# Kernel optimization log

Hardware: AMD Instinct MI355X
Metric: run time of the kernel (lower is better)

Reference implementation:

```python
import jax, jax.numpy as jnp
import numpy as np

N_ACC = 100000   # accounts
N_TX = 300000    # transactions
E = 600000       # edges per edge type
H = 256          # hidden_dim
TX_IN = 32
ACC_IN = 16
L = 2            # conv_layers
M = 300000       # edges to classify
BN_EPS = 1e-5


def setup_inputs() -> dict:
    key = jax.random.key(0)
    ks = jax.random.split(key, 24)
    def nrm(k, shape, scale=1.0):
        return jax.random.normal(k, shape, jnp.float32) * scale
    inp = {}
    inp["x_acc"] = nrm(ks[0], (N_ACC, ACC_IN))
    inp["x_tx"] = nrm(ks[1], (N_TX, TX_IN))
    inp["tx_raw"] = nrm(ks[2], (M, TX_IN))
    # edge type account -> transaction (row0: src account, row1: dst transaction)
    inp["ei_sends"] = jnp.stack([jax.random.randint(ks[3], (E,), 0, N_ACC),
                                 jax.random.randint(ks[4], (E,), 0, N_TX)])
    # edge type transaction -> account
    inp["ei_recv"] = jnp.stack([jax.random.randint(ks[5], (E,), 0, N_TX),
                                jax.random.randint(ks[6], (E,), 0, N_ACC)])
    inp["sender_idx"] = jax.random.randint(ks[7], (M,), 0, N_ACC)
    inp["receiver_idx"] = jax.random.randint(ks[8], (M,), 0, N_ACC)
    # input projections (torch Linear: y = x @ W.T + b)
    inp["W_acc"] = nrm(ks[9], (H, ACC_IN), ACC_IN ** -0.5)
    inp["b_acc"] = jnp.zeros((H,), jnp.float32)
    inp["W_tx"] = nrm(ks[10], (H, TX_IN), TX_IN ** -0.5)
    inp["b_tx"] = jnp.zeros((H,), jnp.float32)
    s = H ** -0.5
    # SAGEConv params per layer: _at = acc->tx edge type, _ta = tx->acc edge type
    # Wl: applied to mean-aggregated neighbor messages (has bias), Wr: root/self weight (no bias)
    inp["Wl_at"] = nrm(ks[11], (L, H, H), s); inp["bl_at"] = jnp.zeros((L, H), jnp.float32)
    inp["Wr_at"] = nrm(ks[12], (L, H, H), s)
    inp["Wl_ta"] = nrm(ks[13], (L, H, H), s); inp["bl_ta"] = jnp.zeros((L, H), jnp.float32)
    inp["Wr_ta"] = nrm(ks[14], (L, H, H), s)
    # shared BatchNorm1d per layer (inference mode: running stats)
    inp["bn_gamma"] = jnp.ones((L, H), jnp.float32)
    inp["bn_beta"] = jnp.zeros((L, H), jnp.float32)
    inp["bn_mean"] = nrm(ks[15], (L, H), 0.1)
    inp["bn_var"] = jax.random.uniform(ks[16], (L, H), jnp.float32, 0.5, 1.5)
    # edge MLP: Linear(2H+TX_IN -> H), ReLU, Linear(H -> 1)
    inp["W1"] = nrm(ks[17], (H, 2 * H + TX_IN), (2 * H + TX_IN) ** -0.5)
    inp["b1"] = jnp.zeros((H,), jnp.float32)
    inp["W2"] = nrm(ks[18], (1, H), s)
    inp["b2"] = jnp.zeros((1,), jnp.float32)
    return inp


def _sage(x_src, x_dst, ei, Wl, bl, Wr):
    # PyG SAGEConv: lin_l(mean_{j in N(i)} x_src[j]) + lin_r(x_dst[i])
    src, dst = ei[0], ei[1]
    n_dst = x_dst.shape[0]
    msg = x_src[src]                                                   # [E, H] gather
    agg = jax.ops.segment_sum(msg, dst, num_segments=n_dst)           # [N_dst, H] scatter-add
    cnt = jax.ops.segment_sum(jnp.ones((ei.shape[1],), x_src.dtype), dst, num_segments=n_dst)
    mean = agg / jnp.maximum(cnt, 1.0)[:, None]
    return mean @ Wl.T + bl + x_dst @ Wr.T


def _bn(v, g, b, m, var):
    return (v - m) * (g * jax.lax.rsqrt(var + BN_EPS)) + b


def reference(x_acc, x_tx, tx_raw, ei_sends, ei_recv, sender_idx, receiver_idx,
              W_acc, b_acc, W_tx, b_tx,
              Wl_at, bl_at, Wr_at, Wl_ta, bl_ta, Wr_ta,
              bn_gamma, bn_beta, bn_mean, bn_var,
              W1, b1, W2, b2):
    acc = jax.nn.relu(x_acc @ W_acc.T + b_acc)
    tx = jax.nn.relu(x_tx @ W_tx.T + b_tx)
    for l in range(L):
        # HeteroConv(aggr='sum'): each node type receives from exactly one edge type here
        tx_new = _sage(acc, tx, ei_sends, Wl_at[l], bl_at[l], Wr_at[l])
        acc_new = _sage(tx, acc, ei_recv, Wl_ta[l], bl_ta[l], Wr_ta[l])
        acc = jax.nn.relu(_bn(acc_new, bn_gamma[l], bn_beta[l], bn_mean[l], bn_var[l]))
        tx = jax.nn.relu(_bn(tx_new, bn_gamma[l], bn_beta[l], bn_mean[l], bn_var[l]))
    h_sender = acc[sender_idx]      # [M, H]
    h_receiver = acc[receiver_idx]  # [M, H]
    edge_repr = jnp.concatenate([h_sender, h_receiver, tx_raw], axis=1)  # [M, 2H+TX_IN]
    h = jax.nn.relu(edge_repr @ W1.T + b1)
    return (h @ W2.T + b2)[:, 0]    # [M]
```

## Files before the change

### kernel.cpp

```cpp
#include <hip/hip_runtime.h>
#include <hip/hip_bf16.h>

#define H 256
#define NACC 100000
#define NTX  300000
#define NE   600000
#define NM   300000

typedef unsigned short u16;
typedef unsigned int u32;
typedef __bf16 bf16x8 __attribute__((ext_vector_type(8)));
typedef float f32x4 __attribute__((ext_vector_type(4)));

__device__ __forceinline__ float bf2f(u32 u) {
    union { u32 i; float f; } v; v.i = u << 16; return v.f;
}
__device__ __forceinline__ u16 f2bf(float f) {
    union { float f; u32 i; } v; v.f = f;
    u32 r = v.i + 0x7FFFu + ((v.i >> 16) & 1u);
    return (u16)(r >> 16);
}
__device__ __forceinline__ u32 pk2(float a, float b) {
    return (u32)f2bf(a) | ((u32)f2bf(b) << 16);
}

__global__ void fillz_kernel(u32* __restrict__ p, long long n) {
    long long i = (long long)blockIdx.x * blockDim.x + threadIdx.x;
    long long st = (long long)gridDim.x * blockDim.x;
    for (; i < n; i += st) p[i] = 0u;
}

__global__ void wcat_kernel(const float* __restrict__ Wl, const float* __restrict__ Wr,
                            u16* __restrict__ dst) {
    int c = blockIdx.x, t = threadIdx.x;
    dst[(size_t)c * 512 + t]       = f2bf(Wl[(size_t)c * 256 + t]);
    dst[(size_t)c * 512 + 256 + t] = f2bf(Wr[(size_t)c * 256 + t]);
}
__global__ void wcat_frag_kernel(const float* __restrict__ Wl, const float* __restrict__ Wr,
                                 u16* __restrict__ dst) {
    int c = blockIdx.x, k = threadIdx.x;
    float v = (k < 256) ? Wl[(size_t)c * 256 + k] : Wr[(size_t)c * 256 + (k - 256)];
    int kstep = k >> 5, kg = (k & 31) >> 3, j = k & 7;
    dst[(size_t)((kstep * 16 + (c >> 4)) * 64 + kg * 16 + (c & 15)) * 8 + j] = f2bf(v);
}
__global__ void w1frag_kernel(const float* __restrict__ W1, u16* __restrict__ dst) {
    int c = blockIdx.x;
    for (int k = threadIdx.x; k < 544; k += 256) {
        float v = W1[(size_t)c * 544 + k];
        int kstep = k >> 5, kg = (k & 31) >> 3, j = k & 7;
        dst[(size_t)((kstep * 16 + (c >> 4)) * 64 + kg * 16 + (c & 15)) * 8 + j] = f2bf(v);
    }
}
__global__ void wproj_kernel(const float* __restrict__ W, u16* __restrict__ dst, int K) {
    int c = blockIdx.x, t = threadIdx.x;
    dst[(size_t)c * 32 + t] = (t < K) ? f2bf(W[(size_t)c * K + t]) : (u16)0;
}
__global__ void bnprep_kernel(const float* __restrict__ bl, const float* __restrict__ g,
                              const float* __restrict__ be, const float* __restrict__ m,
                              const float* __restrict__ v,
                              float* __restrict__ S, float* __restrict__ B) {
    int c = threadIdx.x;
    float s = g[c] * rsqrtf(v[c] + 1e-5f);
    S[c] = s;
    B[c] = (bl[c] - m[c]) * s + be[c];
}

template <int KK>
__launch_bounds__(256)
__global__ void proj_mfma(const float* __restrict__ x, const u16* __restrict__ Wb,
                          const float* __restrict__ b, u16* __restrict__ out, int N) {
    __shared__ __align__(16) u16 Af[8][64][8];
    __shared__ __align__(16) u16 Bf[16][64][8];
    int tid = threadIdx.x;
    int w = tid >> 6, lane = tid & 63;
    int row0 = blockIdx.x * 128;
    {
        int r = tid >> 1, h = tid & 1;
        int gr = row0 + r;
        int rt = r >> 4, rr = r & 15;
        uint4 p0 = make_uint4(0, 0, 0, 0), p1 = p0;
        if (gr < N && (KK == 32 || h == 0)) {
            const float* xp = x + (size_t)gr * KK + h * 16;
            float4 f0 = *(const float4*)(xp);
            float4 f1 = *(const float4*)(xp + 4);
            float4 f2 = *(const float4*)(xp + 8);
            float4 f3 = *(const float4*)(xp + 12);
            p0 = make_uint4(pk2(f0.x, f0.y), pk2(f0.z, f0.w), pk2(f1.x, f1.y), pk2(f1.z, f1.w));
            p1 = make_uint4(pk2(f2.x, f2.y), pk2(f2.z, f2.w), pk2(f3.x, f3.y), pk2(f3.z, f3.w));
        }
        int kg0 = 2 * h;
        *(uint4*)(&Af[rt][(kg0 * 16 + rr) ^ (kg0 << 2)][0]) = p0;
        *(uint4*)(&Af[rt][((kg0 + 1) * 16 + rr) ^ ((kg0 + 1) << 2)][0]) = p1;
    }
    {
        const u16* wp = Wb + (size_t)tid * 32;
#pragma unroll
        for (int q = 0; q < 4; ++q) {
            uint4 wv = *(const uint4*)(wp + q * 8);
            *(uint4*)(&Bf[tid >> 4][q * 16 + (tid & 15)][0]) = wv;
        }
    }
    __syncthreads();
    int arslot = lane ^ ((lane >> 4) << 2);
    f32x4 acc[8][4];
#pragma unroll
    for (int rt = 0; rt < 8; ++rt) {
        bf16x8 afr = *(const bf16x8*)(&Af[rt][arslot][0]);
#pragma unroll
        for (int ct = 0; ct < 4; ++ct) {
            bf16x8 bfr = *(const bf16x8*)(&Bf[w * 4 + ct][lane][0]);
            acc[rt][ct] = __builtin_amdgcn_mfma_f32_16x16x32_bf16(
                afr, bfr, (f32x4){0.f, 0.f, 0.f, 0.f}, 0, 0, 0);
        }
    }
    int rb = (lane >> 4) * 4, cc = lane & 15;
#pragma unroll
    for (int ct = 0; ct < 4; ++ct) {
        int cg = (w * 4 + ct) * 16 + cc;
        float bv = b[cg];
#pragma unroll
        for (int rt = 0; rt < 8; ++rt)
#pragma unroll
            for (int q = 0; q < 4; ++q) {
                int r = row0 + rt * 16 + rb + q;
                if (r < N)
                    out[(size_t)r * H + cg] = f2bf(fmaxf(acc[rt][ct][q] + bv, 0.0f));
            }
    }
}

__global__ void count_kernel(const int* __restrict__ dst, int E, int* __restrict__ cnt) {
    int e = blockIdx.x * blockDim.x + threadIdx.x;
    if (e < E) atomicAdd(&cnt[dst[e]], 1);
}
__global__ void scan1_kernel(const int* __restrict__ cnt, int N,
                             int* __restrict__ loc, int* __restrict__ bsum) {
    __shared__ int sh[256];
    int b = blockIdx.x, t = threadIdx.x;
    int base = b * 1024 + t * 4;
    int v0 = (base + 0 < N) ? cnt[base + 0] : 0;
    int v1 = (base + 1 < N) ? cnt[base + 1] : 0;
    int v2 = (base + 2 < N) ? cnt[base + 2] : 0;
    int v3 = (base + 3 < N) ? cnt[base + 3] : 0;
    int s = v0 + v1 + v2 + v3;
    sh[t] = s;
    __syncthreads();
    for (int o = 1; o < 256; o <<= 1) {
        int y = (t >= o) ? sh[t - o] : 0;
        __syncthreads();
        sh[t] += y;
        __syncthreads();
    }
    int run = sh[t] - s;
    if (base + 0 < N) loc[base + 0] = run; run += v0;
    if (base + 1 < N) loc[base + 1] = run; run += v1;
    if (base + 2 < N) loc[base + 2] = run; run += v2;
    if (base + 3 < N) loc[base + 3] = run;
    if (t == 0) bsum[b] = sh[255];
}
__global__ void scan2_kernel(int* __restrict__ bsum, int nb) {
    __shared__ int sh[1024];
    int t = threadIdx.x;
    int v = (t < nb) ? bsum[t] : 0;
    sh[t] = v;
    __syncthreads();
    for (int o = 1; o < 1024; o <<= 1) {
        int y = (t >= o) ? sh[t - o] : 0;
        __syncthreads();
        sh[t] += y;
        __syncthreads();
    }
    if (t < nb) bsum[t] = sh[t] - v;
}
__global__ void scan3_kernel(int* __restrict__ ptr, const int* __restrict__ bsum,
                             int N, int total) {
    int i = blockIdx.x * blockDim.x + threadIdx.x;
    if (i < N) ptr[i] += bsum[i >> 10];
    else if (i == N) ptr[N] = total;
}
__global__ void fillcsr_kernel(const int* __restrict__ src, const int* __restrict__ dst, int E,
                               const int* __restrict__ ptr, int* __restrict__ cur,
                               int* __restrict__ perm) {
    int e = blockIdx.x * blockDim.x + threadIdx.x;
    if (e < E) {
        int d = dst[e];
        int pos = ptr[d] + atomicAdd(&cur[d], 1);
        perm[pos] = src[e];
    }
}

template <int WS>
__launch_bounds__(256)
__global__ void gmean_kernel(const u16* __restrict__ feat, int fstride,
                             const int* __restrict__ ptr, const int* __restrict__ perm,
                             u16* __restrict__ out, int ostride, int c0,
                             int rows, int lo) {
    constexpr int LPD = WS / 4;
    constexpr int DPB = 256 / LPD;
    int g = threadIdx.x / LPD;
    int ln = threadIdx.x % LPD;
    int w = blockIdx.x * DPB + g;
    if (w >= rows) return;
    int d = lo + w;
    int e0 = ptr[d], e1 = ptr[d + 1];
    float a0 = 0.f, a1 = 0.f, a2 = 0.f, a3 = 0.f;
    for (int e = e0; e < e1; ++e) {
        int s = perm[e];
        uint2 v = *(const uint2*)(feat + (size_t)s * fstride + (ln << 2));
        a0 += bf2f(v.x & 0xffff); a1 += bf2f(v.x >> 16);
        a2 += bf2f(v.y & 0xffff); a3 += bf2f(v.y >> 16);
    }
    int deg = e1 - e0;
    float sc = (deg > 0) ? (1.0f / (float)deg) : 0.0f;
    uint2 pk;
    pk.x = pk2(a0 * sc, a1 * sc);
    pk.y = pk2(a2 * sc, a3 * sc);
    *(uint2*)(out + (size_t)w * ostride + c0 + (ln << 2)) = pk;
}

template <int K, int NC>
__launch_bounds__(256)
__global__ void proj2_kernel(const float* __restrict__ x, const float* __restrict__ W,
                             const float* __restrict__ b, u16* __restrict__ out,
                             int N, int c0, int ost) {
    __shared__ float xs[128][K + 4];
    constexpr int NG = 512 / NC;
    constexpr int RPT = 128 / NG;
    int tid = threadIdx.x;
    int row0 = blockIdx.x * 128;
    constexpr int NF4 = 128 * K / 4;
    for (int f = tid; f < NF4; f += 256) {
        int r = f / (K / 4), kq = (f % (K / 4)) * 4;
        int gr = row0 + r;
        float4 v = (gr < N) ? *(const float4*)(x + (size_t)gr * K + kq)
                            : make_float4(0.f, 0.f, 0.f, 0.f);
        *(float4*)&xs[r][kq] = v;
    }
    int lt2 = (tid % (NC / 2)) * 2;
    int g = tid / (NC / 2);
    float wa[K], wb[K];
    const float* wpa = W + (size_t)(c0 + lt2) * K;
#pragma unroll
    for (int k = 0; k < K; k += 4) {
        float4 va = *(const float4*)(wpa + k);
        float4 vb = *(const float4*)(wpa + K + k);
        wa[k] = va.x; wa[k + 1] = va.y; wa[k + 2] = va.z; wa[k + 3] = va.w;
        wb[k] = vb.x; wb[k + 1] = vb.y; wb[k + 2] = vb.z; wb[k + 3] = vb.w;
    }
    float b0 = b[c0 + lt2], b1 = b[c0 + lt2 + 1];
    __syncthreads();
#pragma unroll
    for (int rr = 0; rr < RPT; ++rr) {
        int r = g * RPT + rr;
        int gr = row0 + r;
        float a0 = b0, a1 = b1;
#pragma unroll
        for (int k = 0; k < K; k += 4) {
            float4 xv = *(const float4*)&xs[r][k];
            a0 += xv.x * wa[k] + xv.y * wa[k + 1] + xv.z * wa[k + 2] + xv.w * wa[k + 3];
            a1 += xv.x * wb[k] + xv.y * wb[k + 1] + xv.z * wb[k + 2] + xv.w * wb[k + 3];
        }
        if (gr < N) {
            u32 pk = (u32)f2bf(fmaxf(a0, 0.f)) | ((u32)f2bf(fmaxf(a1, 0.f)) << 16);
            *(u32*)(out + (size_t)gr * ost + lt2) = pk;
        }
    }
}

__launch_bounds__(256)
__global__ void combine_gather(const u16* __restrict__ featG, const int* __restrict__ ptr,
                               const int* __restrict__ perm, const u16* __restrict__ xd,
                               const u16* __restrict__ WcF,
                               const float* __restrict__ bnS, const float* __restrict__ bnB,
                               u16* __restrict__ outF, int rows) {
    __shared__ __align__(16) u16 Am[8][4][64][8];
    int tid = threadIdx.x;
    int w = tid >> 6, lane = tid & 63;
    int row0 = blockIdx.x * 64;

    {
        int r = tid >> 2, g = tid & 3;
        int grow = row0 + r;
        float s[64];
#pragma unroll
        for (int i = 0; i < 64; ++i) s[i] = 0.0f;
        float inv = 0.0f;
        if (grow < rows) {
            int e0 = ptr[grow], e1 = ptr[grow + 1];
            int dg = e1 - e0;
            inv = (dg > 0) ? 1.0f / (float)dg : 0.0f;
            int e = e0;
            for (; e + 1 < e1; e += 2) {
                int n0 = perm[e], n1 = perm[e + 1];
                const u16* p0 = featG + (size_t)n0 * H + g * 64;
                const u16* p1 = featG + (size_t)n1 * H + g * 64;
#pragma unroll
                for (int q = 0; q < 8; ++q) {
                    uint4 v0 = *(const uint4*)(p0 + q * 8);
                    uint4 v1 = *(const uint4*)(p1 + q * 8);
                    s[q * 8 + 0] += bf2f(v0.x & 0xffff) + bf2f(v1.x & 0xffff);
                    s[q * 8 + 1] += bf2f(v0.x >> 16)    + bf2f(v1.x >> 16);
                    s[q * 8 + 2] += bf2f(v0.y & 0xffff) + bf2f(v1.y & 0xffff);
                    s[q * 8 + 3] += bf2f(v0.y >> 16)    + bf2f(v1.y >> 16);
                    s[q * 8 + 4] += bf2f(v0.z & 0xffff) + bf2f(v1.z & 0xffff);
                    s[q * 8 + 5] += bf2f(v0.z >> 16)    + bf2f(v1.z >> 16);
                    s[q * 8 + 6] += bf2f(v0.w & 0xffff) + bf2f(v1.w & 0xffff);
                    s[q * 8 + 7] += bf2f(v0.w >> 16)    + bf2f(v1.w >> 16);
                }
            }
            if (e < e1) {
                int n0 = perm[e];
                const u16* p0 = featG + (size_t)n0 * H + g * 64;
#pragma unroll
                for (int q = 0; q < 8; ++q) {
                    uint4 v0 = *(const uint4*)(p0 + q * 8);
                    s[q * 8 + 0] += bf2f(v0.x & 0xffff);
                    s[q * 8 + 1] += bf2f(v0.x >> 16);
                    s[q * 8 + 2] += bf2f(v0.y & 0xffff);
                    s[q * 8 + 3] += bf2f(v0.y >> 16);
                    s[q * 8 + 4] += bf2f(v0.z & 0xffff);
                    s[q * 8 + 5] += bf2f(v0.z >> 16);
                    s[q * 8 + 6] += bf2f(v0.w & 0xffff);
                    s[q * 8 + 7] += bf2f(v0.w >> 16);
                }
            }
        }
        int rt = r >> 4, rr = r & 15;
#pragma unroll
        for (int q = 0; q < 8; ++q) {
            int kgg = g * 8 + q;
            int kbs = kgg >> 2, akg = kgg & 3;
            uint4 pv;
            pv.x = pk2(s[q * 8 + 0] * inv, s[q * 8 + 1] * inv);
            pv.y = pk2(s[q * 8 + 2] * inv, s[q * 8 + 3] * inv);
            pv.z = pk2(s[q * 8 + 4] * inv, s[q * 8 + 5] * inv);
            pv.w = pk2(s[q * 8 + 6] * inv, s[q * 8 + 7] * inv);
            *(uint4*)(&Am[kbs][rt][(akg * 16 + rr) ^ (akg << 2)][0]) = pv;
        }
    }
    __syncthreads();

    int arslot = lane ^ ((lane >> 4) << 2);
    const u16* xrow[4];
#pragma unroll
    for (int rt = 0; rt < 4; ++rt) {
        int r = row0 + rt * 16 + (lane & 15);
        if (r > rows - 1) r = rows - 1;
        xrow[rt] = xd + (size_t)r * H + (lane >> 4) * 8;
    }
    const u16* wbase = WcF + (size_t)(w * 4) * 512 + (size_t)lane * 8;

    f32x4 acc[4][4];
#pragma unroll
    for (int i = 0; i < 4; ++i)
#pragma unroll
        for (int j = 0; j < 4; ++j) acc[i][j] = (f32x4){0.f, 0.f, 0.f, 0.f};

#pragma unroll 4
    for (int kb = 0; kb < 512; kb += 32) {
        int kstep = kb >> 5;
        bf16x8 afr[4];
        if (kb < 256) {
#pragma unroll
            for (int rt = 0; rt < 4; ++rt)
                afr[rt] = *(const bf16x8*)(&Am[kstep][rt][arslot][0]);
        } else {
#pragma unroll
            for (int rt = 0; rt < 4; ++rt)
                afr[rt] = *(const bf16x8*)(xrow[rt] + (kb - 256));
        }
#pragma unroll
        for (int ct = 0; ct < 4; ++ct) {
            bf16x8 bfr = *(const bf16x8*)(wbase + (size_t)(kstep * 16 + ct) * 512);
#pragma unroll
            for (int rt = 0; rt < 4; ++rt)
                acc[rt][ct] = __builtin_amdgcn_mfma_f32_16x16x32_bf16(afr[rt], bfr, acc[rt][ct], 0, 0, 0);
        }
    }
    __syncthreads();
    int rb = (lane >> 4) * 4, cc = lane & 15;
#pragma unroll
    for (int ct = 0; ct < 4; ++ct) {
        int cg = (w * 4 + ct) * 16 + cc;
        float s = bnS[cg], sh = bnB[cg];
#pragma unroll
        for (int rt = 0; rt < 4; ++rt)
#pragma unroll
            for (int q = 0; q < 4; ++q) {
                int r = row0 + rt * 16 + rb + q;
                if (r < rows)
                    outF[(size_t)r * H + cg] = f2bf(fmaxf(acc[rt][ct][q] * s + sh, 0.0f));
            }
    }
}

template <int COLS>
__launch_bounds__(256)
__global__ void combine_mfma(const u16* __restrict__ mean_, const u16* __restrict__ xd,
                             const u16* __restrict__ Wcat,
                             const float* __restrict__ bnS, const float* __restrict__ bnB,
                             u16* __restrict__ outF, int ostride, int out_c0,
                             int rows, int c0) {
    constexpr int NCT = COLS / 16;
    constexpr int CTW = NCT / 4;
    constexpr int PPT = (COLS * 4) / 256;
    __shared__ __align__(16) u16 Af[4][64][8];
    __shared__ __align__(16) u16 Bf[NCT][64][8];
    int tid = threadIdx.x;
    int w = tid >> 6, lane = tid & 63;
    int row0 = blockIdx.x * 64;
    int arow = tid >> 2, akg = tid & 3;
    bool arok = (row0 + arow) < rows;
    const u16* am = mean_ + (size_t)(row0 + arow) * H;
    const u16* ax = xd + (size_t)(row0 + arow) * H;
    int awslot = (akg * 16 + (arow & 15)) ^ (akg << 2);
    int arslot = lane ^ ((lane >> 4) << 2);
    int bc = tid % COLS;
    int bkg0 = (tid / COLS) * PPT;
    const u16* wp0 = Wcat + (size_t)(c0 + bc) * 512 + bkg0 * 8;

    f32x4 acc[4][CTW];
#pragma unroll
    for (int i = 0; i < 4; ++i)
#pragma unroll
        for (int j = 0; j < CTW; ++j) acc[i][j] = (f32x4){0.f, 0.f, 0.f, 0.f};

    for (int kb = 0; kb < 512; kb += 32) {
        uint4 av = make_uint4(0, 0, 0, 0);
        if (arok) {
            int kg = kb + akg * 8;
            av = (kg < 256) ? *(const uint4*)(am + kg) : *(const uint4*)(ax + (kg - 256));
        }
        *(uint4*)(&Af[arow >> 4][awslot][0]) = av;
#pragma unroll
        for (int q = 0; q < PPT; ++q) {
            uint4 wv = *(const uint4*)(wp0 + kb + q * 8);
            *(uint4*)(&Bf[bc >> 4][(bkg0 + q) * 16 + (bc & 15)][0]) = wv;
        }
        __syncthreads();
        bf16x8 afr[4];
#pragma unroll
        for (int rt = 0; rt < 4; ++rt)
            afr[rt] = *(const bf16x8*)(&Af[rt][arslot][0]);
#pragma unroll
        for (int ctl = 0; ctl < CTW; ++ctl) {
            bf16x8 b = *(const bf16x8*)(&Bf[w * CTW + ctl][lane][0]);
#pragma unroll
            for (int rt = 0; rt < 4; ++rt)
                acc[rt][ctl] = __builtin_amdgcn_mfma_f32_16x16x32_bf16(afr[rt], b, acc[rt][ctl], 0, 0, 0);
        }
        __syncthreads();
    }
    int rb = (lane >> 4) * 4;
    int ccol = lane & 15;
#pragma unroll
    for (int ctl = 0; ctl < CTW; ++ctl) {
        int clocal = (w * CTW + ctl) * 16 + ccol;
        int cg = c0 + clocal;
        float s = bnS[cg], sh = bnB[cg];
#pragma unroll
        for (int rt = 0; rt < 4; ++rt) {
#pragma unroll
            for (int q = 0; q < 4; ++q) {
                int r = row0 + rt * 16 + rb + q;
                if (r < rows)
                    outF[(size_t)r * ostride + out_c0 + clocal] = f2bf(fmaxf(acc[rt][ctl][q] * s + sh, 0.0f));
            }
        }
    }
}

__launch_bounds__(256)
__global__ void mlp_mfma(const u16* __restrict__ accF, const int* __restrict__ sidx,
                         const int* __restrict__ ridx, const float* __restrict__ txr,
                         const u16* __restrict__ W1F, const float* __restrict__ b1,
                         const float* __restrict__ W2, const float* __restrict__ b2,
                         float* __restrict__ out, int M) {
    __shared__ __align__(16) u16 Af[4][64][8];
    __shared__ float red[4][64];
    int tid = threadIdx.x;
    int w = tid >> 6, lane = tid & 63;
    int row0 = blockIdx.x * 64;
    int arow = tid >> 2, akg = tid & 3;
    int grow = row0 + arow;
    bool arok = grow < M;
    int si = arok ? sidx[grow] : 0;
    int ri = arok ? ridx[grow] : 0;
    int awslot = (akg * 16 + (arow & 15)) ^ (akg << 2);
    int arslot = lane ^ ((lane >> 4) << 2);
    const u16* wbase = W1F + (size_t)(w * 4) * 512 + (size_t)lane * 8;

    f32x4 acc[4][4];
#pragma unroll
    for (int i = 0; i < 4; ++i)
#pragma unroll
        for (int j = 0; j < 4; ++j) acc[i][j] = (f32x4){0.f, 0.f, 0.f, 0.f};

    for (int kb = 0; kb < 544; kb += 32) {
        uint4 av = make_uint4(0, 0, 0, 0);
        if (arok) {
            int kg = kb + akg * 8;
            if (kg < 256) av = *(const uint4*)(accF + (size_t)si * H + kg);
            else if (kg < 512) av = *(const uint4*)(accF + (size_t)ri * H + (kg - 256));
            else {
                float4 f0 = *(const float4*)(txr + (size_t)grow * 32 + (kg - 512));
                float4 f1 = *(const float4*)(txr + (size_t)grow * 32 + (kg - 512) + 4);
                av.x = pk2(f0.x, f0.y); av.y = pk2(f0.z, f0.w);
                av.z = pk2(f1.x, f1.y); av.w = pk2(f1.z, f1.w);
            }
        }
        *(uint4*)(&Af[arow >> 4][awslot][0]) = av;
        __syncthreads();
        int kstep = kb >> 5;
        bf16x8 afr[4];
#pragma unroll
        for (int rt = 0; rt < 4; ++rt)
            afr[rt] = *(const bf16x8*)(&Af[rt][arslot][0]);
#pragma unroll
        for (int ct = 0; ct < 4; ++ct) {
            bf16x8 bfr = *(const bf16x8*)(wbase + (size_t)(kstep * 16 + ct) * 512);
#pragma unroll
            for (int rt = 0; rt < 4; ++rt)
                acc[rt][ct] = __builtin_amdgcn_mfma_f32_16x16x32_bf16(afr[rt], bfr, acc[rt][ct], 0, 0, 0);
        }
        __syncthreads();
    }
    float part[4][4];
#pragma unroll
    for (int rt = 0; rt < 4; ++rt)
#pragma unroll
        for (int q = 0; q < 4; ++q) part[rt][q] = 0.0f;
#pragma unroll
    for (int ct = 0; ct < 4; ++ct) {
        int cg = (w * 4 + ct) * 16 + (lane & 15);
        float b1v = b1[cg], w2v = W2[cg];
#pragma unroll
        for (int rt = 0; rt < 4; ++rt)
#pragma unroll
            for (int q = 0; q < 4; ++q)
                part[rt][q] += fmaxf(acc[rt][ct][q] + b1v, 0.0f) * w2v;
    }
    int rb = (lane >> 4) * 4;
#pragma unroll
    for (int rt = 0; rt < 4; ++rt)
#pragma unroll
        for (int q = 0; q < 4; ++q) {
            float p = part[rt][q];
            p += __shfl_xor(p, 1);
            p += __shfl_xor(p, 2);
            p += __shfl_xor(p, 4);
            p += __shfl_xor(p, 8);
            if ((lane & 15) == 0) red[w][rt * 16 + rb + q] = p;
        }
    __syncthreads();
    if (tid < 64) {
        int r = row0 + tid;
        if (r < M)
            out[r] = red[0][tid] + red[1][tid] + red[2][tid] + red[3][tid] + b2[0];
    }
}

static inline void fz(void* p, size_t bytes, hipStream_t s) {
    long long n = (long long)(bytes >> 2);
    int g = (int)(((n + 255) / 256 < 2048) ? (n + 255) / 256 : 2048);
    fillz_kernel<<<g, 256, 0, s>>>((u32*)p, n);
}
static inline size_t al256(size_t x) { return (x + 255) & ~(size_t)255; }

extern "C" void kernel_launch(void* const* d_in, const int* in_sizes, int n_in,
                              void* d_out, int out_size, void* d_ws, size_t ws_size,
                              hipStream_t stream) {
    const float* x_acc  = (const float*)d_in[0];
    const float* x_tx   = (const float*)d_in[1];
    const float* tx_raw = (const float*)d_in[2];
    const int* ei_sends = (const int*)d_in[3];
    const int* ei_recv  = (const int*)d_in[4];
    const int* sidx     = (const int*)d_in[5];
    const int* ridx     = (const int*)d_in[6];
    const float* W_acc  = (const float*)d_in[7];
    const float* b_acc  = (const float*)d_in[8];
    const float* W_tx   = (const float*)d_in[9];
    const float* b_tx   = (const float*)d_in[10];
    const float* Wl_at  = (const float*)d_in[11];
    const float* bl_at  = (const float*)d_in[12];
    const float* Wr_at  = (const float*)d_in[13];
    const float* Wl_ta  = (const float*)d_in[14];
    const float* bl_ta  = (const float*)d_in[15];
    const float* Wr_ta  = (const float*)d_in[16];
    const float* bng    = (const float*)d_in[17];
    const float* bnb    = (const float*)d_in[18];
    const float* bnm    = (const float*)d_in[19];
    const float* bnv    = (const float*)d_in[20];
    const float* W1     = (const float*)d_in[21];
    const float* b1     = (const float*)d_in[22];
    const float* W2     = (const float*)d_in[23];
    const float* b2     = (const float*)d_in[24];
    float* out = (float*)d_out;

    const size_t szFeatA = (size_t)NACC * H * 2;
    const size_t szFeatT = (size_t)NTX * H * 2;
    const size_t szCSR = al256((NTX + 1) * 4) + al256(4096) + al256((NTX + 1) * 4)
                       + al256((size_t)NE * 4) + al256((NACC + 1) * 4) + al256((size_t)NE * 4);
    const size_t szW = 3 * al256(256 * 512 * 2) + 3 * al256(16 * 16 * 64 * 8 * 2)
                     + al256(17 * 16 * 64 * 8 * 2)
                     + 2 * al256(3 * 256 * 4) + 2 * al256(256 * 32 * 2);

    size_t needF = szCSR + szW + 2 * al256(szFeatA) + al256(szFeatT) + 65536;
    auto needS = [&](int S, int CC) {
        return 3 * al256(szFeatA) + szCSR + szW + 2 * al256((size_t)CC * H * 2)
             + al256((size_t)NTX * (H / S) * 2) + 65536;
    };
    int plan, S = 2, CC = 16384;
    if (needF <= ws_size)                { plan = 0; }
    else if (needS(2, 16384) <= ws_size) { plan = 1; S = 2; CC = 16384; }
    else if (needS(4, 16384) <= ws_size) { plan = 1; S = 4; CC = 16384; }
    else                                 { plan = 1; S = 4; CC = 2048; }

    char* wsp = (char*)d_ws;
    size_t off = 0;
    auto alloc = [&](size_t bytes) -> void* {
        void* p = wsp + off;
        off = al256(off + bytes);
        return p;
    };
    int* cnt   = (int*)alloc((NTX + 1) * 4);
    int* bsum  = (int*)alloc(4096);
    int* ptrT  = (int*)alloc((NTX + 1) * 4);
    int* permS = (int*)alloc((size_t)NE * 4);
    int* ptrA  = (int*)alloc((NACC + 1) * 4);
    int* permR = (int*)alloc((size_t)NE * 4);
    u16* Wc[3];
    Wc[0] = (u16*)alloc(256 * 512 * 2);
    Wc[1] = (u16*)alloc(256 * 512 * 2);
    Wc[2] = (u16*)alloc(256 * 512 * 2);
    u16* WcF[3];
    WcF[0] = (u16*)alloc(16 * 16 * 64 * 8 * 2);
    WcF[1] = (u16*)alloc(16 * 16 * 64 * 8 * 2);
    WcF[2] = (u16*)alloc(16 * 16 * 64 * 8 * 2);
    u16* W1F = (u16*)alloc(17 * 16 * 64 * 8 * 2);
    float* bnS = (float*)alloc(3 * 256 * 4);
    float* bnB = (float*)alloc(3 * 256 * 4);
    u16* WbA = (u16*)alloc(256 * 32 * 2);
    u16* WbT = (u16*)alloc(256 * 32 * 2);
    u16* A0f = (u16*)alloc(szFeatA);
    u16* A1f = (u16*)alloc(szFeatA);

    wcat_kernel<<<256, 256, 0, stream>>>(Wl_ta, Wr_ta, Wc[0]);
    wcat_kernel<<<256, 256, 0, stream>>>(Wl_at, Wr_at, Wc[1]);
    wcat_kernel<<<256, 256, 0, stream>>>(Wl_ta + H * H, Wr_ta + H * H, Wc[2]);
    wcat_frag_kernel<<<256, 512, 0, stream>>>(Wl_ta, Wr_ta, WcF[0]);
    wcat_frag_kernel<<<256, 512, 0, stream>>>(Wl_at, Wr_at, WcF[1]);
    wcat_frag_kernel<<<256, 512, 0, stream>>>(Wl_ta + H * H, Wr_ta + H * H, WcF[2]);
    w1frag_kernel<<<256, 256, 0, stream>>>(W1, W1F);
    wproj_kernel<<<256, 32, 0, stream>>>(W_acc, WbA, 16);
    wproj_kernel<<<256, 32, 0, stream>>>(W_tx, WbT, 32);
    bnprep_kernel<<<1, 256, 0, stream>>>(bl_ta, bng, bnb, bnm, bnv, bnS, bnB);
    bnprep_kernel<<<1, 256, 0, stream>>>(bl_at, bng, bnb, bnm, bnv, bnS + 256, bnB + 256);
    bnprep_kernel<<<1, 256, 0, stream>>>(bl_ta + H, bng + H, bnb + H, bnm + H, bnv + H,
                                         bnS + 512, bnB + 512);

    const int EG = (NE + 255) / 256;
    const int nbT = (NTX + 1023) / 1024, nbA = (NACC + 1023) / 1024;
    fz(cnt, (size_t)NTX * 4, stream);
    count_kernel<<<EG, 256, 0, stream>>>(ei_sends + NE, NE, cnt);
    scan1_kernel<<<nbT, 256, 0, stream>>>(cnt, NTX, ptrT, bsum);
    scan2_kernel<<<1, 1024, 0, stream>>>(bsum, nbT);
    scan3_kernel<<<(NTX + 256) / 256 + 1, 256, 0, stream>>>(ptrT, bsum, NTX, NE);
    fz(cnt, (size_t)NTX * 4, stream);
    fillcsr_kernel<<<EG, 256, 0, stream>>>(ei_sends, ei_sends + NE, NE, ptrT, cnt, permS);
    fz(cnt, (size_t)NACC * 4, stream);
    count_kernel<<<EG, 256, 0, stream>>>(ei_recv + NE, NE, cnt);
    scan1_kernel<<<nbA, 256, 0, stream>>>(cnt, NACC, ptrA, bsum);
    scan2_kernel<<<1, 1024, 0, stream>>>(bsum, nbA);
    scan3_kernel<<<(NACC + 256) / 256 + 1, 256, 0, stream>>>(ptrA, bsum, NACC, NE);
    fz(cnt, (size_t)NACC * 4, stream);
    fillcsr_kernel<<<EG, 256, 0, stream>>>(ei_recv, ei_recv + NE, NE, ptrA, cnt, permR);

    proj_mfma<16><<<(NACC + 127) / 128, 256, 0, stream>>>(x_acc, WbA, b_acc, A0f, NACC);

    const int gA = (NACC + 63) / 64, gM = (NM + 63) / 64;

    if (plan == 0) {
        u16* T = (u16*)alloc(szFeatT);
        proj_mfma<32><<<(NTX + 127) / 128, 256, 0, stream>>>(x_tx, WbT, b_tx, T, NTX);
        combine_gather<<<gA, 256, 0, stream>>>(T, ptrA, permR, A0f, WcF[0], bnS, bnB, A1f, NACC);
        combine_gather<<<(NTX + 63) / 64, 256, 0, stream>>>(A0f, ptrT, permS, T, WcF[1],
                                                            bnS + 256, bnB + 256, T, NTX);
        combine_gather<<<gA, 256, 0, stream>>>(T, ptrA, permR, A1f, WcF[2],
                                               bnS + 512, bnB + 512, A0f, NACC);
        mlp_mfma<<<gM, 256, 0, stream>>>(A0f, sidx, ridx, tx_raw, W1F, b1, W2, b2, out, NM);
    } else {
        u16* meanbuf = (u16*)alloc(szFeatA);
        u16* T0c     = (u16*)alloc((size_t)CC * H * 2);
        u16* meanTc  = (u16*)alloc((size_t)CC * H * 2);
        const int WSL = H / S;
        u16* Tslice  = (u16*)alloc((size_t)NTX * WSL * 2);

        for (int s = 0; s < S; ++s) {
            int c0 = s * WSL;
            if (WSL == 128)
                proj2_kernel<32, 128><<<(NTX + 127) / 128, 256, 0, stream>>>(x_tx, W_tx, b_tx, Tslice, NTX, c0, WSL);
            else
                proj2_kernel<32, 64><<<(NTX + 127) / 128, 256, 0, stream>>>(x_tx, W_tx, b_tx, Tslice, NTX, c0, WSL);
            if (WSL == 128)
                gmean_kernel<128><<<(NACC + 7) / 8, 256, 0, stream>>>(Tslice, WSL, ptrA, permR, meanbuf, H, c0, NACC, 0);
            else
                gmean_kernel<64><<<(NACC + 15) / 16, 256, 0, stream>>>(Tslice, WSL, ptrA, permR, meanbuf, H, c0, NACC, 0);
        }
        combine_mfma<256><<<gA, 256, 0, stream>>>(meanbuf, A0f, Wc[0], bnS, bnB, A1f, H, 0, NACC, 0);
        for (int s = 0; s < S; ++s) {
            int c0 = s * WSL;
            for (int lo = 0; lo < NTX; lo += CC) {
                int cur = (NTX - lo < CC) ? (NTX - lo) : CC;
                proj2_kernel<32, 256><<<(cur + 127) / 128, 256, 0, stream>>>(x_tx + (size_t)lo * 32, W_tx, b_tx, T0c, cur, 0, H);
                gmean_kernel<256><<<(cur + 3) / 4, 256, 0, stream>>>(A0f, H, ptrT, permS, meanTc, H, 0, cur, lo);
                if (WSL == 128)
                    combine_mfma<128><<<(cur + 63) / 64, 256, 0, stream>>>(
                        meanTc, T0c, Wc[1], bnS + 256, bnB + 256,
                        Tslice + (size_t)lo * WSL, WSL, 0, cur, c0);
                else
                    combine_mfma<64><<<(cur + 63) / 64, 256, 0, stream>>>(
                        meanTc, T0c, Wc[1], bnS + 256, bnB + 256,
                        Tslice + (size_t)lo * WSL, WSL, 0, cur, c0);
            }
            if (WSL == 128)
                gmean_kernel<128><<<(NACC + 7) / 8, 256, 0, stream>>>(Tslice, WSL, ptrA, permR, meanbuf, H, c0, NACC, 0);
            else
                gmean_kernel<64><<<(NACC + 15) / 16, 256, 0, stream>>>(Tslice, WSL, ptrA, permR, meanbuf, H, c0, NACC, 0);
        }
        combine_mfma<256><<<gA, 256, 0, stream>>>(meanbuf, A1f, Wc[2], bnS + 512, bnB + 512, A0f, H, 0, NACC, 0);
        mlp_mfma<<<gM, 256, 0, stream>>>(A0f, sidx, ridx, tx_raw, W1F, b1, W2, b2, out, NM);
    }
}
```

Before: 1.088 ms.

## Double block size in gather-combine and MLP kernels, loading A fragments directly

combine_gather and mlp_mfma now run with 512 threads per block. Each wave covers 2 column tiles instead of 4, and each gather thread accumulates 32 features instead of 64, which cuts register pressure and doubles the number of threads issuing gather loads. mlp_mfma drops its per-k-step LDS staging and barriers and loads A fragments straight from global memory through per-row pointers. The trade-off is that weight fragments are loaded by twice as many waves per block, and the uncoalesced direct gathers in the MLP may use cache less well.

```diff
diff --git a/kernel.cpp b/kernel.cpp
--- a/kernel.cpp
+++ b/kernel.cpp
@@ -22,6 +22,12 @@
 }
 __device__ __forceinline__ u32 pk2(float a, float b) {
     return (u32)f2bf(a) | ((u32)f2bf(b) << 16);
+}
+__device__ __forceinline__ void acc8(float* s, uint4 v) {
+    s[0] += bf2f(v.x & 0xffff); s[1] += bf2f(v.x >> 16);
+    s[2] += bf2f(v.y & 0xffff); s[3] += bf2f(v.y >> 16);
+    s[4] += bf2f(v.z & 0xffff); s[5] += bf2f(v.z >> 16);
+    s[6] += bf2f(v.w & 0xffff); s[7] += bf2f(v.w >> 16);
 }
 
 __global__ void fillz_kernel(u32* __restrict__ p, long long n) {
@@ -267,7 +273,7 @@
     }
 }
 
-__launch_bounds__(256)
+__launch_bounds__(512)
 __global__ void combine_gather(const u16* __restrict__ featG, const int* __restrict__ ptr,
                                const int* __restrict__ perm, const u16* __restrict__ xd,
                                const u16* __restrict__ WcF,
@@ -279,11 +285,11 @@
     int row0 = blockIdx.x * 64;
 
     {
-        int r = tid >> 2, g = tid & 3;
+        int r = tid >> 3, g = tid & 7;
         int grow = row0 + r;
-        float s[64];
-#pragma unroll
-        for (int i = 0; i < 64; ++i) s[i] = 0.0f;
+        float s[32];
+#pragma unroll
+        for (int i = 0; i < 32; ++i) s[i] = 0.0f;
         float inv = 0.0f;
         if (grow < rows) {
             int e0 = ptr[grow], e1 = ptr[grow + 1];
@@ -292,43 +298,28 @@
             int e = e0;
             for (; e + 1 < e1; e += 2) {
                 int n0 = perm[e], n1 = perm[e + 1];
-                const u16* p0 = featG + (size_t)n0 * H + g * 64;
-                const u16* p1 = featG + (size_t)n1 * H + g * 64;
-#pragma unroll
-                for (int q = 0; q < 8; ++q) {
+                const u16* p0 = featG + (size_t)n0 * H + g * 32;
+                const u16* p1 = featG + (size_t)n1 * H + g * 32;
+#pragma unroll
+                for (int q = 0; q < 4; ++q) {
                     uint4 v0 = *(const uint4*)(p0 + q * 8);
                     uint4 v1 = *(const uint4*)(p1 + q * 8);
-                    s[q * 8 + 0] += bf2f(v0.x & 0xffff) + bf2f(v1.x & 0xffff);
-                    s[q * 8 + 1] += bf2f(v0.x >> 16)    + bf2f(v1.x >> 16);
-                    s[q * 8 + 2] += bf2f(v0.y & 0xffff) + bf2f(v1.y & 0xffff);
-                    s[q * 8 + 3] += bf2f(v0.y >> 16)    + bf2f(v1.y >> 16);
-                    s[q * 8 + 4] += bf2f(v0.z & 0xffff) + bf2f(v1.z & 0xffff);
-                    s[q * 8 + 5] += bf2f(v0.z >> 16)    + bf2f(v1.z >> 16);
-                    s[q * 8 + 6] += bf2f(v0.w & 0xffff) + bf2f(v1.w & 0xffff);
-                    s[q * 8 + 7] += bf2f(v0.w >> 16)    + bf2f(v1.w >> 16);
+                    acc8(s + q * 8, v0);
+                    acc8(s + q * 8, v1);
                 }
             }
             if (e < e1) {
                 int n0 = perm[e];
-                const u16* p0 = featG + (size_t)n0 * H + g * 64;
-#pragma unroll
-                for (int q = 0; q < 8; ++q) {
-                    uint4 v0 = *(const uint4*)(p0 + q * 8);
-                    s[q * 8 + 0] += bf2f(v0.x & 0xffff);
-                    s[q * 8 + 1] += bf2f(v0.x >> 16);
-                    s[q * 8 + 2] += bf2f(v0.y & 0xffff);
-                    s[q * 8 + 3] += bf2f(v0.y >> 16);
-                    s[q * 8 + 4] += bf2f(v0.z & 0xffff);
-                    s[q * 8 + 5] += bf2f(v0.z >> 16);
-                    s[q * 8 + 6] += bf2f(v0.w & 0xffff);
-                    s[q * 8 + 7] += bf2f(v0.w >> 16);
-                }
+                const u16* p0 = featG + (size_t)n0 * H + g * 32;
+#pragma unroll
+                for (int q = 0; q < 4; ++q)
+                    acc8(s + q * 8, *(const uint4*)(p0 + q * 8));
             }
         }
         int rt = r >> 4, rr = r & 15;
 #pragma unroll
-        for (int q = 0; q < 8; ++q) {
-            int kgg = g * 8 + q;
+        for (int q = 0; q < 4; ++q) {
+            int kgg = g * 4 + q;
             int kbs = kgg >> 2, akg = kgg & 3;
             uint4 pv;
             pv.x = pk2(s[q * 8 + 0] * inv, s[q * 8 + 1] * inv);
@@ -348,40 +339,47 @@
         if (r > rows - 1) r = rows - 1;
         xrow[rt] = xd + (size_t)r * H + (lane >> 4) * 8;
     }
-    const u16* wbase = WcF + (size_t)(w * 4) * 512 + (size_t)lane * 8;
-
-    f32x4 acc[4][4];
-#pragma unroll
-    for (int i = 0; i < 4; ++i)
-#pragma unroll
-        for (int j = 0; j < 4; ++j) acc[i][j] = (f32x4){0.f, 0.f, 0.f, 0.f};
-
-#pragma unroll 4
-    for (int kb = 0; kb < 512; kb += 32) {
-        int kstep = kb >> 5;
+    const u16* wb = WcF + (size_t)lane * 8;
+
+    f32x4 acc[4][2];
+#pragma unroll
+    for (int i = 0; i < 4; ++i) {
+        acc[i][0] = (f32x4){0.f, 0.f, 0.f, 0.f};
+        acc[i][1] = (f32x4){0.f, 0.f, 0.f, 0.f};
+    }
+#pragma unroll
+    for (int ks = 0; ks < 8; ++ks) {
         bf16x8 afr[4];
-        if (kb < 256) {
+#pragma unroll
+        for (int rt = 0; rt < 4; ++rt)
+            afr[rt] = *(const bf16x8*)(&Am[ks][rt][arslot][0]);
+#pragma unroll
+        for (int j = 0; j < 2; ++j) {
+            bf16x8 bfr = *(const bf16x8*)(wb + (size_t)(ks * 16 + w * 2 + j) * 512);
 #pragma unroll
             for (int rt = 0; rt < 4; ++rt)
-                afr[rt] = *(const bf16x8*)(&Am[kstep][rt][arslot][0]);
-        } else {
+                acc[rt][j] = __builtin_amdgcn_mfma_f32_16x16x32_bf16(afr[rt], bfr, acc[rt][j], 0, 0, 0);
+        }
+    }
+#pragma unroll
+    for (int ks = 8; ks < 16; ++ks) {
+        bf16x8 afr[4];
+#pragma unroll
+        for (int rt = 0; rt < 4; ++rt)
+            afr[rt] = *(const bf16x8*)(xrow[rt] + (ks - 8) * 32);
+#pragma unroll
+        for (int j = 0; j < 2; ++j) {
+            bf16x8 bfr = *(const bf16x8*)(wb + (size_t)(ks * 16 + w * 2 + j) * 512);
 #pragma unroll
             for (int rt = 0; rt < 4; ++rt)
-                afr[rt] = *(const bf16x8*)(xrow[rt] + (kb - 256));
-        }
-#pragma unroll
-        for (int ct = 0; ct < 4; ++ct) {
-            bf16x8 bfr = *(const bf16x8*)(wbase + (size_t)(kstep * 16 + ct) * 512);
-#pragma unroll
-            for (int rt = 0; rt < 4; ++rt)
-                acc[rt][ct] = __builtin_amdgcn_mfma_f32_16x16x32_bf16(afr[rt], bfr, acc[rt][ct], 0, 0, 0);
+                acc[rt][j] = __builtin_amdgcn_mfma_f32_16x16x32_bf16(afr[rt], bfr, acc[rt][j], 0, 0, 0);
         }
     }
     __syncthreads();
     int rb = (lane >> 4) * 4, cc = lane & 15;
 #pragma unroll
-    for (int ct = 0; ct < 4; ++ct) {
-        int cg = (w * 4 + ct) * 16 + cc;
+    for (int j = 0; j < 2; ++j) {
+        int cg = (w * 2 + j) * 16 + cc;
         float s = bnS[cg], sh = bnB[cg];
 #pragma unroll
         for (int rt = 0; rt < 4; ++rt)
@@ -389,7 +387,7 @@
             for (int q = 0; q < 4; ++q) {
                 int r = row0 + rt * 16 + rb + q;
                 if (r < rows)
-                    outF[(size_t)r * H + cg] = f2bf(fmaxf(acc[rt][ct][q] * s + sh, 0.0f));
+                    outF[(size_t)r * H + cg] = f2bf(fmaxf(acc[rt][j][q] * s + sh, 0.0f));
             }
     }
 }
@@ -470,60 +468,81 @@
     }
 }
 
-__launch_bounds__(256)
+__launch_bounds__(512)
 __global__ void mlp_mfma(const u16* __restrict__ accF, const int* __restrict__ sidx,
                          const int* __restrict__ ridx, const float* __restrict__ txr,
                          const u16* __restrict__ W1F, const float* __restrict__ b1,
                          const float* __restrict__ W2, const float* __restrict__ b2,
                          float* __restrict__ out, int M) {
-    __shared__ __align__(16) u16 Af[4][64][8];
-    __shared__ float red[4][64];
+    __shared__ float red[8][64];
     int tid = threadIdx.x;
     int w = tid >> 6, lane = tid & 63;
     int row0 = blockIdx.x * 64;
-    int arow = tid >> 2, akg = tid & 3;
-    int grow = row0 + arow;
-    bool arok = grow < M;
-    int si = arok ? sidx[grow] : 0;
-    int ri = arok ? ridx[grow] : 0;
-    int awslot = (akg * 16 + (arow & 15)) ^ (akg << 2);
-    int arslot = lane ^ ((lane >> 4) << 2);
-    const u16* wbase = W1F + (size_t)(w * 4) * 512 + (size_t)lane * 8;
-
-    f32x4 acc[4][4];
-#pragma unroll
-    for (int i = 0; i < 4; ++i)
-#pragma unroll
-        for (int j = 0; j < 4; ++j) acc[i][j] = (f32x4){0.f, 0.f, 0.f, 0.f};
-
-    for (int kb = 0; kb < 544; kb += 32) {
-        uint4 av = make_uint4(0, 0, 0, 0);
-        if (arok) {
-            int kg = kb + akg * 8;
-            if (kg < 256) av = *(const uint4*)(accF + (size_t)si * H + kg);
-            else if (kg < 512) av = *(const uint4*)(accF + (size_t)ri * H + (kg - 256));
-            else {
-                float4 f0 = *(const float4*)(txr + (size_t)grow * 32 + (kg - 512));
-                float4 f1 = *(const float4*)(txr + (size_t)grow * 32 + (kg - 512) + 4);
-                av.x = pk2(f0.x, f0.y); av.y = pk2(f0.z, f0.w);
-                av.z = pk2(f1.x, f1.y); av.w = pk2(f1.z, f1.w);
-            }
-        }
-        *(uint4*)(&Af[arow >> 4][awslot][0]) = av;
-        __syncthreads();
-        int kstep = kb >> 5;
+    int koff = (lane >> 4) * 8;
+    const u16 *sp[4], *rp[4];
+    const float* tp[4];
+#pragma unroll
+    for (int rt = 0; rt < 4; ++rt) {
+        int r = row0 + rt * 16 + (lane & 15);
+        if (r > M - 1) r = M - 1;
+        sp[rt] = accF + (size_t)sidx[r] * H + koff;
+        rp[rt] = accF + (size_t)ridx[r] * H + koff;
+        tp[rt] = txr + (size_t)r * 32 + koff;
+    }
+    const u16* wb = W1F + (size_t)lane * 8;
+
+    f32x4 acc[4][2];
+#pragma unroll
+    for (int i = 0; i < 4; ++i) {
+        acc[i][0] = (f32x4){0.f, 0.f, 0.f, 0.f};
+        acc[i][1] = (f32x4){0.f, 0.f, 0.f, 0.f};
+    }
+#pragma unroll
+    for (int ks = 0; ks < 8; ++ks) {
         bf16x8 afr[4];
 #pragma unroll
         for (int rt = 0; rt < 4; ++rt)
-            afr[rt] = *(const bf16x8*)(&Af[rt][arslot][0]);
-#pragma unroll
-        for (int ct = 0; ct < 4; ++ct) {
-            bf16x8 bfr = *(const bf16x8*)(wbase + (size_t)(kstep * 16 + ct) * 512);
+            afr[rt] = *(const bf16x8*)(sp[rt] + ks * 32);
+#pragma unroll
+        for (int j = 0; j < 2; ++j) {
+            bf16x8 bfr = *(const bf16x8*)(wb + (size_t)(ks * 16 + w * 2 + j) * 512);
 #pragma unroll
             for (int rt = 0; rt < 4; ++rt)
-                acc[rt][ct] = __builtin_amdgcn_mfma_f32_16x16x32_bf16(afr[rt], bfr, acc[rt][ct], 0, 0, 0);
-        }
-        __syncthreads();
+                acc[rt][j] = __builtin_amdgcn_mfma_f32_16x16x32_bf16(afr[rt], bfr, acc[rt][j], 0, 0, 0);
+        }
+    }
+#pragma unroll
+    for (int ks = 8; ks < 16; ++ks) {
+        bf16x8 afr[4];
+#pragma unroll
+        for (int rt = 0; rt < 4; ++rt)
+            afr[rt] = *(const bf16x8*)(rp[rt] + (ks - 8) * 32);
+#pragma unroll
+        for (int j = 0; j < 2; ++j) {
+            bf16x8 bfr = *(const bf16x8*)(wb + (size_t)(ks * 16 + w * 2 + j) * 512);
+#pragma unroll
+            for (int rt = 0; rt < 4; ++rt)
+                acc[rt][j] = __builtin_amdgcn_mfma_f32_16x16x32_bf16(afr[rt], bfr, acc[rt][j], 0, 0, 0);
+        }
+    }
+    {
+        bf16x8 afr[4];
+#pragma unroll
+        for (int rt = 0; rt < 4; ++rt) {
+            float4 f0 = *(const float4*)(tp[rt]);
+            float4 f1 = *(const float4*)(tp[rt] + 4);
+            uint4 t;
+            t.x = pk2(f0.x, f0.y); t.y = pk2(f0.z, f0.w);
+            t.z = pk2(f1.x, f1.y); t.w = pk2(f1.z, f1.w);
+            afr[rt] = *(const bf16x8*)&t;
+        }
+#pragma unroll
+        for (int j = 0; j < 2; ++j) {
+            bf16x8 bfr = *(const bf16x8*)(wb + (size_t)(16 * 16 + w * 2 + j) * 512);
+#pragma unroll
+            for (int rt = 0; rt < 4; ++rt)
+                acc[rt][j] = __builtin_amdgcn_mfma_f32_16x16x32_bf16(afr[rt], bfr, acc[rt][j], 0, 0, 0);
+        }
     }
     float part[4][4];
 #pragma unroll
@@ -531,14 +550,14 @@
 #pragma unroll
         for (int q = 0; q < 4; ++q) part[rt][q] = 0.0f;
 #pragma unroll
-    for (int ct = 0; ct < 4; ++ct) {
-        int cg = (w * 4 + ct) * 16 + (lane & 15);
+    for (int j = 0; j < 2; ++j) {
+        int cg = (w * 2 + j) * 16 + (lane & 15);
         float b1v = b1[cg], w2v = W2[cg];
 #pragma unroll
         for (int rt = 0; rt < 4; ++rt)
 #pragma unroll
             for (int q = 0; q < 4; ++q)
-                part[rt][q] += fmaxf(acc[rt][ct][q] + b1v, 0.0f) * w2v;
+                part[rt][q] += fmaxf(acc[rt][j][q] + b1v, 0.0f) * w2v;
     }
     int rb = (lane >> 4) * 4;
 #pragma unroll
@@ -556,7 +575,8 @@
     if (tid < 64) {
         int r = row0 + tid;
         if (r < M)
-            out[r] = red[0][tid] + red[1][tid] + red[2][tid] + red[3][tid] + b2[0];
+            out[r] = red[0][tid] + red[1][tid] + red[2][tid] + red[3][tid]
+                   + red[4][tid] + red[5][tid] + red[6][tid] + red[7][tid] + b2[0];
     }
 }
 
@@ -683,12 +703,12 @@
     if (plan == 0) {
         u16* T = (u16*)alloc(szFeatT);
         proj_mfma<32><<<(NTX + 127) / 128, 256, 0, stream>>>(x_tx, WbT, b_tx, T, NTX);
-        combine_gather<<<gA, 256, 0, stream>>>(T, ptrA, permR, A0f, WcF[0], bnS, bnB, A1f, NACC);
-        combine_gather<<<(NTX + 63) / 64, 256, 0, stream>>>(A0f, ptrT, permS, T, WcF[1],
+        combine_gather<<<gA, 512, 0, stream>>>(T, ptrA, permR, A0f, WcF[0], bnS, bnB, A1f, NACC);
+        combine_gather<<<(NTX + 63) / 64, 512, 0, stream>>>(A0f, ptrT, permS, T, WcF[1],
                                                             bnS + 256, bnB + 256, T, NTX);
-        combine_gather<<<gA, 256, 0, stream>>>(T, ptrA, permR, A1f, WcF[2],
+        combine_gather<<<gA, 512, 0, stream>>>(T, ptrA, permR, A1f, WcF[2],
                                                bnS + 512, bnB + 512, A0f, NACC);
-        mlp_mfma<<<gM, 256, 0, stream>>>(A0f, sidx, ridx, tx_raw, W1F, b1, W2, b2, out, NM);
+        mlp_mfma<<<gM, 512, 0, stream>>>(A0f, sidx, ridx, tx_raw, W1F, b1, W2, b2, out, NM);
     } else {
         u16* meanbuf = (u16*)alloc(szFeatA);
         u16* T0c     = (u16*)alloc((size_t)CC * H * 2);
@@ -729,6 +749,6 @@
                 gmean_kernel<64><<<(NACC + 15) / 16, 256, 0, stream>>>(Tslice, WSL, ptrA, permR, meanbuf, H, c0, NACC, 0);
         }
         combine_mfma<256><<<gA, 256, 0, stream>>>(meanbuf, A1f, Wc[2], bnS + 512, bnB + 512, A0f, H, 0, NACC, 0);
-        mlp_mfma<<<gM, 256, 0, stream>>>(A0f, sidx, ridx, tx_raw, W1F, b1, W2, b2, out, NM);
-    }
-}
+        mlp_mfma<<<gM, 512, 0, stream>>>(A0f, sidx, ridx, tx_raw, W1F, b1, W2, b2, out, NM);
+    }
+}
```

Result: slower. 1.197 ms (+10.0%).
